# Kernel tuning notes

Hardware: AMD Instinct MI355X
Metric: run time of the kernel (lower is better)

The kernel has to match this reference:

```python
import jax, jax.numpy as jnp
import numpy as np

BS, NQ, DIMS = 4, 6400, 256
NH, NL, NP, NQUEUE = 8, 1, 4, 2


def ms_deform_attn(value, shapes_np, starts_np, loc, attn):
    # value: [B, Nv, H, D]; loc: [B, Nq, H, L, P, 2] in [0,1]; attn: [B, Nq, H, L, P]
    B, Nv, H, D = value.shape
    _, Nq, _, L, P, _ = loc.shape
    out = jnp.zeros((B, H, Nq, D), loc.dtype)
    for l in range(L):
        Hl, Wl = int(shapes_np[l, 0]), int(shapes_np[l, 1])
        s = int(starts_np[l])
        vl = value[:, s:s + Hl * Wl].transpose(0, 2, 1, 3)  # [B,H,HW,D]
        # grid_sample align_corners=False pixel coords
        x = loc[:, :, :, l, :, 0] * Wl - 0.5  # [B,Nq,H,P]
        y = loc[:, :, :, l, :, 1] * Hl - 0.5
        x0 = jnp.floor(x); y0 = jnp.floor(y)
        dx = x - x0; dy = y - y0
        x0i = x0.astype(jnp.int32); y0i = y0.astype(jnp.int32)
        acc = jnp.zeros((B, H, Nq * P, D), loc.dtype)
        corners = [(x0i, y0i, (1 - dx) * (1 - dy)),
                   (x0i + 1, y0i, dx * (1 - dy)),
                   (x0i, y0i + 1, (1 - dx) * dy),
                   (x0i + 1, y0i + 1, dx * dy)]
        for xi, yi, w in corners:
            valid = (xi >= 0) & (xi < Wl) & (yi >= 0) & (yi < Hl)
            idx = jnp.clip(yi, 0, Hl - 1) * Wl + jnp.clip(xi, 0, Wl - 1)  # [B,Nq,H,P]
            idx_t = idx.transpose(0, 2, 1, 3).reshape(B, H, Nq * P, 1)
            g = jnp.take_along_axis(vl, idx_t, axis=2)  # [B,H,Nq*P,D]
            wv = jnp.where(valid, w, 0.0).transpose(0, 2, 1, 3).reshape(B, H, Nq * P, 1)
            acc = acc + g * wv
        acc = acc.reshape(B, H, Nq, P, D)
        wl = attn[:, :, :, l].transpose(0, 2, 1, 3)  # [B,H,Nq,P]
        out = out + jnp.einsum('bhnpd,bhnp->bhnd', acc, wl)
    return out.transpose(0, 2, 1, 3).reshape(B, Nq, H * D)


def setup_inputs() -> dict:
    key = jax.random.key(0)
    ks = jax.random.split(key, 12)
    d2 = DIMS * NQUEUE
    noff = NQUEUE * NH * NL * NP * 2
    nattn = NQUEUE * NH * NL * NP
    sc = 1.0 / np.sqrt(DIMS)
    return {
        'query': jax.random.normal(ks[0], (BS, NQ, DIMS), jnp.float32),
        'voxbev': jax.random.normal(ks[1], (BS, NQ, DIMS), jnp.float32),
        'reference_points': jax.random.uniform(ks[2], (BS * NQUEUE, NQ, NL, 2), jnp.float32),
        'spatial_shapes': jnp.array([[80, 80]], dtype=jnp.int64),
        'level_start_index': jnp.array([0], dtype=jnp.int64),
        'Wv': jax.random.normal(ks[3], (DIMS, DIMS), jnp.float32) * sc,
        'bv': jax.random.normal(ks[4], (DIMS,), jnp.float32) * 0.01,
        'Woff': jax.random.normal(ks[5], (d2, noff), jnp.float32) * (1.0 / np.sqrt(d2)),
        'boff': jax.random.normal(ks[6], (noff,), jnp.float32),
        'Wattn': jax.random.normal(ks[7], (d2, nattn), jnp.float32) * (1.0 / np.sqrt(d2)),
        'battn': jax.random.normal(ks[8], (nattn,), jnp.float32) * 0.01,
        'Wo': jax.random.normal(ks[9], (DIMS, DIMS), jnp.float32) * sc,
        'bo': jax.random.normal(ks[10], (DIMS,), jnp.float32) * 0.01,
    }


def reference(query, voxbev, reference_points, spatial_shapes, level_start_index,
              Wv, bv, Woff, boff, Wattn, battn, Wo, bo):
    bs, nq, dims = query.shape
    shapes_np = np.asarray(spatial_shapes)
    starts_np = np.asarray(level_start_index)
    identity = query
    # value = stack([query, voxbev], 1).reshape(bs*2, nq, dims) -> interleaved [q0,v0,q1,v1,...]
    value = jnp.stack([query, voxbev], 1).reshape(bs * NQUEUE, nq, dims)
    qcat = jnp.concatenate([value[:bs], query], -1)  # [bs, nq, 2*dims]
    v = (value @ Wv + bv).reshape(bs * NQUEUE, nq, NH, dims // NH)
    off = (qcat @ Woff + boff).reshape(bs, nq, NH, NQUEUE, NL, NP, 2)
    attn = (qcat @ Wattn + battn).reshape(bs, nq, NH, NQUEUE, NL * NP)
    attn = jax.nn.softmax(attn, axis=-1).reshape(bs, nq, NH, NQUEUE, NL, NP)
    attn = attn.transpose(0, 3, 1, 2, 4, 5).reshape(bs * NQUEUE, nq, NH, NL, NP)
    off = off.transpose(0, 3, 1, 2, 4, 5, 6).reshape(bs * NQUEUE, nq, NH, NL, NP, 2)
    # offset normalizer: (W, H) per level
    norm = jnp.stack([spatial_shapes[:, 1], spatial_shapes[:, 0]], -1).astype(off.dtype)  # [L,2]
    loc = reference_points[:, :, None, :, None, :] + off / norm[None, None, None, :, None, :]
    out = ms_deform_attn(v, shapes_np, starts_np, loc, attn)  # [bs*2, nq, dims]
    out = out.reshape(bs, NQUEUE, nq, dims).mean(1)  # mean over queue
    out = out @ Wo + bo
    return out + identity  # dropout is identity in eval
```

## Files before the change

kernel.cpp:

```cpp
#include <hip/hip_runtime.h>
#include <hip/hip_bf16.h>

#define BS   4
#define NQ   6400
#define DIMS 256
#define NH   8
#define NP   4
#define GW   80
#define GH   80

typedef __hip_bfloat16 bf16;
typedef unsigned short ushort;
typedef __attribute__((ext_vector_type(8))) short short8;
typedef __attribute__((ext_vector_type(4))) float floatx4;

union bfu { bf16 h; ushort s; };
__device__ __forceinline__ ushort f2bs(float x) { bfu u; u.h = __float2bfloat16(x); return u.s; }
__device__ __forceinline__ float bs2f(ushort s) { return __uint_as_float(((unsigned)s) << 16); }
__device__ __forceinline__ float ldin(const void* p, size_t i, int isf) {
    return isf ? ((const float*)p)[i] : bs2f(((const ushort*)p)[i]);
}

__device__ __forceinline__ int self_detect(const ushort* __restrict__ q, int tid) {
    int bad = 0;
    const uint4 u0 = ((const uint4*)q)[tid * 2];
    const uint4 u1 = ((const uint4*)q)[tid * 2 + 1];
    const unsigned w[8] = { u0.x, u0.y, u0.z, u0.w, u1.x, u1.y, u1.z, u1.w };
    #pragma unroll
    for (int j = 0; j < 8; ++j) {
        if (((w[j] >> 7)  & 0xFF) > 160) bad = 1;
        if (((w[j] >> 23) & 0xFF) > 160) bad = 1;
    }
    return __any(bad) ? 1 : 0;
}

__global__ __launch_bounds__(256) void prep_k(
    const void* __restrict__ Wv, const void* __restrict__ bv,
    const void* __restrict__ Woff, const void* __restrict__ boff,
    const void* __restrict__ Wattn, const void* __restrict__ battn,
    const void* __restrict__ Wo, const void* __restrict__ bo,
    int* __restrict__ flagp,
    ushort* __restrict__ WvT, ushort* __restrict__ WoaT, ushort* __restrict__ WoT,
    float* __restrict__ biasv, float* __restrict__ biasoa, float* __restrict__ biaso,
    const void* __restrict__ query, const void* __restrict__ voxbev,
    uint4* __restrict__ qb, uint4* __restrict__ vbv)
{
    const int tid = threadIdx.x;
    const int isf = self_detect((const ushort*)query, tid);
    const int bid = blockIdx.x;
    if (bid == 0 && tid == 0) *flagp = isf;
    if (bid < 899) {
        const int i = bid * 256 + tid;
        const int n1 = 256 * 256, n2 = n1 + 192 * 512, n3 = n2 + 256 * 256;
        const int n4 = n3 + 256, n5 = n4 + 192, n6 = n5 + 256;
        if (i < n1) {
            int n = i >> 8, k = i & 255;
            WvT[i] = f2bs(ldin(Wv, (size_t)k * 256 + n, isf));
        } else if (i < n2) {
            int j = i - n1, n = j >> 9, k = j & 511;
            float v = (n < 128) ? ldin(Woff, (size_t)k * 128 + n, isf)
                                : ldin(Wattn, (size_t)k * 64 + (n - 128), isf);
            WoaT[j] = f2bs(v);
        } else if (i < n3) {
            int j = i - n2, n = j >> 8, k = j & 255;
            WoT[j] = f2bs(ldin(Wo, (size_t)k * 256 + n, isf));
        } else if (i < n4) {
            biasv[i - n3] = ldin(bv, i - n3, isf);
        } else if (i < n5) {
            int j = i - n4;
            biasoa[j] = (j < 128) ? ldin(boff, j, isf) : ldin(battn, j - 128, isf);
        } else if (i < n6) {
            biaso[i - n5] = ldin(bo, i - n5, isf);
        }
    } else {
        if (isf == 0) return;
        const int t = (bid - 899) * 256 + tid;
        const int half = 819200;
        const void* src = (t < half) ? query : voxbev;
        uint4* dst = (t < half) ? qb : vbv;
        const int j = (t < half) ? t : t - half;
        const float4* s = (const float4*)src + (size_t)j * 2;
        float4 a = s[0], b = s[1];
        uint4 o;
        o.x = ((unsigned)f2bs(a.y) << 16) | f2bs(a.x);
        o.y = ((unsigned)f2bs(a.w) << 16) | f2bs(a.z);
        o.z = ((unsigned)f2bs(b.y) << 16) | f2bs(b.x);
        o.w = ((unsigned)f2bs(b.w) << 16) | f2bs(b.z);
        dst[j] = o;
    }
}

enum { A_VAL = 0, A_QCAT = 1, A_PLAIN = 2 };
enum { O_BF16 = 0, O_FINAL = 1, O_VPERM = 2, O_OAPERM = 3 };

#define SROW 264
#define APAD 40
#define CST  67
#define SMEMB (64 * SROW * 2 + 2 * 128 * APAD * 2)

template <int AMODE, int OMODE, int KTOT, int NX, int MG>
__device__ __forceinline__ void pgemm_body(
    const int F, char* smem,
    const ushort* __restrict__ Apl, const ushort* __restrict__ BT,
    const float* __restrict__ biasf, void* __restrict__ C,
    const void* __restrict__ query_raw, const void* __restrict__ voxbev_raw,
    const ushort* __restrict__ qb, const ushort* __restrict__ vbv,
    const int isf)
{
    constexpr int N = NX * 64;
    constexpr int NPH = KTOT / 256;
    short* pan = (short*)smem;
    short* ap0 = (short*)(smem + 64 * SROW * 2);
    short* ap1 = ap0 + 128 * APAD;
    float* cbf = (float*)smem;

    const int xcd = F & 7, l = F >> 3;
    const int n = l % NX;
    const int mg = (l / NX) * 8 + xcd;
    if (mg >= MG) return;
    const int bm = mg * 128, bn = n * 64;

    const int tid = threadIdx.x;
    const int lane = tid & 63, wv = tid >> 6;
    const int wm = wv * 32;
    const int fr = lane & 15, fq = (lane >> 4) * 8;
    const int arow = tid >> 1, acs = (tid & 1) * 16;

    const ushort* qsrc = isf ? qb  : (const ushort*)query_raw;
    const ushort* vsrc = isf ? vbv : (const ushort*)voxbev_raw;
    const ushort* aph[NPH];
    if (AMODE == A_PLAIN) {
        aph[0] = Apl + (size_t)bm * DIMS;
    } else {
        const int b = bm / NQ, q0 = bm - (bm / NQ) * NQ;
        aph[0] = ((b & 1) ? vsrc : qsrc) + (size_t)((b >> 1) * NQ + q0) * DIMS;
        if (AMODE == A_QCAT) aph[1] = qsrc + (size_t)(b * NQ + q0) * DIMS;
    }

    floatx4 acc[2][4] = {};

    for (int ph = 0; ph < NPH; ++ph) {
        #pragma unroll
        for (int i = 0; i < 8; ++i) {
            const int c = tid * 8 + i;
            const int row = c >> 5, j = (c & 31) * 8;
            *(uint4*)&pan[row * SROW + j] =
                *(const uint4*)&BT[(size_t)(bn + row) * KTOT + ph * 256 + j];
        }
        const ushort* ab = aph[ph];
        {
            uint4 s0 = *(const uint4*)&ab[(size_t)arow * DIMS + acs];
            uint4 s1 = *(const uint4*)&ab[(size_t)arow * DIMS + acs + 8];
            *(uint4*)&ap0[arow * APAD + acs] = s0;
            *(uint4*)&ap0[arow * APAD + acs + 8] = s1;
        }
        __syncthreads();

        #pragma unroll
        for (int t = 0; t < 8; ++t) {
            const short* acur = (t & 1) ? ap1 : ap0;
            short* anxt = (t & 1) ? ap0 : ap1;
            uint4 s0, s1;
            if (t < 7) {
                s0 = *(const uint4*)&ab[(size_t)arow * DIMS + (t + 1) * 32 + acs];
                s1 = *(const uint4*)&ab[(size_t)arow * DIMS + (t + 1) * 32 + acs + 8];
            }
            short8 af[2], bf[4];
            #pragma unroll
            for (int mt = 0; mt < 2; ++mt)
                af[mt] = *(const short8*)&acur[(wm + mt * 16 + fr) * APAD + fq];
            #pragma unroll
            for (int nt = 0; nt < 4; ++nt)
                bf[nt] = *(const short8*)&pan[(nt * 16 + fr) * SROW + t * 32 + fq];
            #pragma unroll
            for (int mt = 0; mt < 2; ++mt)
                #pragma unroll
                for (int nt = 0; nt < 4; ++nt)
                    acc[mt][nt] = __builtin_amdgcn_mfma_f32_16x16x32_bf16(
                        af[mt], bf[nt], acc[mt][nt], 0, 0, 0);
            if (t < 7) {
                *(uint4*)&anxt[arow * APAD + acs] = s0;
                *(uint4*)&anxt[arow * APAD + acs + 8] = s1;
            }
            __syncthreads();
        }
    }

    const int col = lane & 15, rq = (lane >> 4) * 4;
    #pragma unroll
    for (int mt = 0; mt < 2; ++mt)
        #pragma unroll
        for (int nt = 0; nt < 4; ++nt)
            #pragma unroll
            for (int r = 0; r < 4; ++r)
                cbf[(wm + mt * 16 + rq + r) * CST + nt * 16 + col] = acc[mt][nt][r];
    __syncthreads();

    if (OMODE == O_FINAL && isf) {
        const int r16 = tid >> 4, cc = tid & 15;
        #pragma unroll
        for (int it = 0; it < 8; ++it) {
            const int lr = it * 16 + r16;
            const size_t g = (size_t)(bm + lr);
            float4 x = *(const float4*)&cbf[lr * CST + cc * 4];
            const ushort* rs = qsrc + g * DIMS + bn + cc * 4;
            x.x += biasf[bn + cc * 4 + 0] + bs2f(rs[0]);
            x.y += biasf[bn + cc * 4 + 1] + bs2f(rs[1]);
            x.z += biasf[bn + cc * 4 + 2] + bs2f(rs[2]);
            x.w += biasf[bn + cc * 4 + 3] + bs2f(rs[3]);
            *(float4*)((float*)C + g * N + bn + cc * 4) = x;
        }
    } else {
        const int r8 = tid >> 3, c8 = tid & 7;
        #pragma unroll
        for (int it = 0; it < 4; ++it) {
            const int lr = it * 32 + r8;
            const size_t g = (size_t)(bm + lr);
            float4 x0 = *(const float4*)&cbf[lr * CST + c8 * 8];
            float4 x1 = *(const float4*)&cbf[lr * CST + c8 * 8 + 4];
            float xs[8] = { x0.x, x0.y, x0.z, x0.w, x1.x, x1.y, x1.z, x1.w };
            #pragma unroll
            for (int e = 0; e < 8; ++e) xs[e] += biasf[bn + c8 * 8 + e];
            if (OMODE == O_FINAL) {
                const ushort* rs = qsrc + g * DIMS + bn + c8 * 8;
                #pragma unroll
                for (int e = 0; e < 8; ++e) xs[e] += bs2f(rs[e]);
            }
            uint4 o;
            o.x = ((unsigned)f2bs(xs[1]) << 16) | f2bs(xs[0]);
            o.y = ((unsigned)f2bs(xs[3]) << 16) | f2bs(xs[2]);
            o.z = ((unsigned)f2bs(xs[5]) << 16) | f2bs(xs[4]);
            o.w = ((unsigned)f2bs(xs[7]) << 16) | f2bs(xs[6]);
            ushort* dstp;
            if (OMODE == O_VPERM) {
                const int cc = bn + c8 * 8;
                const int s = (int)(g / NQ), qq = (int)(g % NQ);
                dstp = (ushort*)C + ((size_t)(s * 8 + (cc >> 5)) * NQ + qq) * 32
                                  + (cc & 31);
            } else if (OMODE == O_OAPERM) {
                const int cc = bn + c8 * 8;
                const int bb = (int)(g / NQ), qq = (int)(g % NQ);
                int hh, off;
                if (cc < 128) { hh = cc >> 4; off = cc & 15; }
                else          { hh = (cc - 128) >> 3; off = 16; }
                dstp = (ushort*)C + ((size_t)(bb * 8 + hh) * NQ + qq) * 24 + off;
            } else {
                dstp = (ushort*)C + g * N + bn + c8 * 8;
            }
            *(uint4*)dstp = o;
        }
    }
}

__global__ __launch_bounds__(256) void gemm12_k(
    const ushort* __restrict__ WvT, const float* __restrict__ biasv,
    ushort* __restrict__ v_ws,
    const ushort* __restrict__ WoaT, const float* __restrict__ biasoa,
    ushort* __restrict__ offraw,
    const void* __restrict__ query_raw, const void* __restrict__ voxbev_raw,
    const ushort* __restrict__ qb, const ushort* __restrict__ vbv,
    const int* __restrict__ flagp)
{
    __shared__ __align__(16) char smem[SMEMB];
    const int isf = *flagp;
    const int bid = blockIdx.x;
    if (bid < 1600) {
        pgemm_body<A_VAL, O_VPERM, 256, 4, 400>(bid, smem,
            nullptr, WvT, biasv, (void*)v_ws, query_raw, voxbev_raw, qb, vbv, isf);
    } else {
        pgemm_body<A_QCAT, O_OAPERM, 512, 3, 200>(bid - 1600, smem,
            nullptr, WoaT, biasoa, (void*)offraw, query_raw, voxbev_raw, qb, vbv, isf);
    }
}

__global__ __launch_bounds__(256) void gemm4_k(
    const ushort* __restrict__ Apl, const ushort* __restrict__ BT,
    const float* __restrict__ biasf, void* __restrict__ C,
    const void* __restrict__ query_raw, const void* __restrict__ voxbev_raw,
    const ushort* __restrict__ qb, const ushort* __restrict__ vbv,
    const int* __restrict__ flagp)
{
    __shared__ __align__(16) char smem[SMEMB];
    const int isf = *flagp;
    pgemm_body<A_PLAIN, O_FINAL, 256, 4, 200>(blockIdx.x, smem,
        Apl, BT, biasf, C, query_raw, voxbev_raw, qb, vbv, isf);
}

__global__ __launch_bounds__(256) void sample_k(
    const ushort* __restrict__ v,
    const ushort* __restrict__ offp,
    const void* __restrict__ refpts,
    const int* __restrict__ flagp,
    ushort* __restrict__ sampled)
{
    const int isf = *flagp;
    __shared__ int   sidx[64][2][17];
    __shared__ float swt [64][2][17];
    const int tid = threadIdx.x;
    const int j = blockIdx.x;
    const int h = j & 7;
    const int k = j >> 3;
    const int b = k / 100;
    const int q0 = (k % 100) * 64;

    if (tid < 128) {
        const int lq = tid >> 1, queue = tid & 1;
        const int q = q0 + lq;
        const ushort* rec = offp + ((size_t)(b * 8 + h) * NQ + q) * 24;
        const ushort* al = rec + 16 + queue * 4;
        float l0 = bs2f(al[0]), l1 = bs2f(al[1]), l2 = bs2f(al[2]), l3 = bs2f(al[3]);
        float mx = fmaxf(fmaxf(l0, l1), fmaxf(l2, l3));
        float e0 = __expf(l0 - mx), e1 = __expf(l1 - mx);
        float e2 = __expf(l2 - mx), e3 = __expf(l3 - mx);
        float inv = 0.5f / (e0 + e1 + e2 + e3);
        const int bq = b * 2 + queue;
        const float rx = ldin(refpts, ((size_t)bq * NQ + q) * 2 + 0, isf);
        const float ry = ldin(refpts, ((size_t)bq * NQ + q) * 2 + 1, isf);
        const ushort* od = rec + queue * 8;
        float ww[4] = { e0 * inv, e1 * inv, e2 * inv, e3 * inv };
        #pragma unroll
        for (int p = 0; p < NP; ++p) {
            const float x = rx * (float)GW + bs2f(od[p * 2 + 0]) - 0.5f;
            const float y = ry * (float)GH + bs2f(od[p * 2 + 1]) - 0.5f;
            const float x0f = floorf(x), y0f = floorf(y);
            const float dx = x - x0f, dy = y - y0f;
            const int x0 = (int)x0f, y0 = (int)y0f;
            const float wp = ww[p];
            const float cw4[4] = { wp * (1.0f - dx) * (1.0f - dy),
                                   wp * dx * (1.0f - dy),
                                   wp * (1.0f - dx) * dy,
                                   wp * dx * dy };
            #pragma unroll
            for (int c = 0; c < 4; ++c) {
                const int xs = x0 + (c & 1), ys = y0 + (c >> 1);
                const bool ok = (unsigned)xs < (unsigned)GW && (unsigned)ys < (unsigned)GH;
                const int xi = min(max(xs, 0), GW - 1);
                const int yi = min(max(ys, 0), GH - 1);
                sidx[lq][queue][p * 4 + c] = yi * GW + xi;
                swt [lq][queue][p * 4 + c] = ok ? cw4[c] : 0.0f;
            }
        }
    }
    __syncthreads();

    const int lq = tid >> 2, d8 = tid & 3;
    const int q = q0 + lq;
    float a[8] = {};
    #pragma unroll
    for (int queue = 0; queue < 2; ++queue) {
        const ushort* vb = v + (((size_t)(b * 2 + queue) * 8 + h) * NQ) * 32 + d8 * 8;
        #pragma unroll
        for (int hf = 0; hf < 2; ++hf) {
            uint4 g[8];
            #pragma unroll
            for (int u = 0; u < 8; ++u) {
                const int ci = sidx[lq][queue][hf * 8 + u];
                g[u] = *(const uint4*)&vb[(size_t)ci * 32];
            }
            __builtin_amdgcn_sched_barrier(0);
            #pragma unroll
            for (int u = 0; u < 8; ++u) {
                const float cw = swt[lq][queue][hf * 8 + u];
                a[0] += cw * bs2f((ushort)g[u].x); a[1] += cw * bs2f((ushort)(g[u].x >> 16));
                a[2] += cw * bs2f((ushort)g[u].y); a[3] += cw * bs2f((ushort)(g[u].y >> 16));
                a[4] += cw * bs2f((ushort)g[u].z); a[5] += cw * bs2f((ushort)(g[u].z >> 16));
                a[6] += cw * bs2f((ushort)g[u].w); a[7] += cw * bs2f((ushort)(g[u].w >> 16));
            }
        }
    }
    uint4 o;
    o.x = ((unsigned)f2bs(a[1]) << 16) | f2bs(a[0]);
    o.y = ((unsigned)f2bs(a[3]) << 16) | f2bs(a[2]);
    o.z = ((unsigned)f2bs(a[5]) << 16) | f2bs(a[4]);
    o.w = ((unsigned)f2bs(a[7]) << 16) | f2bs(a[6]);
    *(uint4*)&sampled[((size_t)b * NQ + q) * DIMS + h * 32 + d8 * 8] = o;
}

extern "C" void kernel_launch(void* const* d_in, const int* in_sizes, int n_in,
                              void* d_out, int out_size, void* d_ws, size_t ws_size,
                              hipStream_t stream)
{
    const void* query  = d_in[0];
    const void* voxbev = d_in[1];
    const void* refpts = d_in[2];
    const void* Wv   = d_in[5];  const void* bv    = d_in[6];
    const void* Woff = d_in[7];  const void* boff  = d_in[8];
    const void* Wattn= d_in[9];  const void* battn = d_in[10];
    const void* Wo   = d_in[11]; const void* bo    = d_in[12];

    char* p = (char*)d_ws;
    int* flag = (int*)p;             p += 256;
    ushort* WvT  = (ushort*)p;       p += 256 * 256 * 2;
    ushort* WoaT = (ushort*)p;       p += 192 * 512 * 2;
    ushort* WoT  = (ushort*)p;       p += 256 * 256 * 2;
    float* biasv  = (float*)p;       p += 1024;
    float* biasoa = (float*)p;       p += 1024;
    float* biaso  = (float*)p;       p += 1024;
    ushort* qb   = (ushort*)p;       p += (size_t)BS * NQ * DIMS * 2;
    ushort* vbv  = (ushort*)p;       p += (size_t)BS * NQ * DIMS * 2;
    ushort* v_ws = (ushort*)p;       p += (size_t)2 * BS * NQ * DIMS * 2;
    ushort* offraw = (ushort*)p;     p += (size_t)BS * NQ * 192 * 2;
    ushort* sampled = (ushort*)p;

    prep_k<<<7299, 256, 0, stream>>>(Wv, bv, Woff, boff, Wattn, battn, Wo, bo,
                                     flag, WvT, WoaT, WoT, biasv, biasoa, biaso,
                                     query, voxbev, (uint4*)qb, (uint4*)vbv);

    gemm12_k<<<2200, 256, 0, stream>>>(WvT, biasv, v_ws, WoaT, biasoa, offraw,
                                       query, voxbev, qb, vbv, flag);

    sample_k<<<3200, 256, 0, stream>>>(v_ws, offraw, refpts, flag, sampled);

    gemm4_k<<<800, 256, 0, stream>>>(sampled, WoT, biaso, d_out,
                                     query, voxbev, qb, vbv, flag);
}
```

Before: 209.7 us.

## Load GEMM tiles directly to LDS with XOR-swizzled layout and larger K tiles

```diff
diff --git a/kernel.cpp b/kernel.cpp
--- a/kernel.cpp
+++ b/kernel.cpp
@@ -19,6 +19,13 @@
 __device__ __forceinline__ float bs2f(ushort s) { return __uint_as_float(((unsigned)s) << 16); }
 __device__ __forceinline__ float ldin(const void* p, size_t i, int isf) {
     return isf ? ((const float*)p)[i] : bs2f(((const ushort*)p)[i]);
+}
+
+__device__ __forceinline__ void gl_lds16(const void* gsrc, void* ldst) {
+    __builtin_amdgcn_global_load_lds(
+        (const __attribute__((address_space(1))) unsigned int*)gsrc,
+        (__attribute__((address_space(3))) unsigned int*)ldst,
+        16, 0, 0);
 }
 
 __device__ __forceinline__ int self_detect(const ushort* __restrict__ q, int tid) {
@@ -93,10 +100,11 @@
 enum { A_VAL = 0, A_QCAT = 1, A_PLAIN = 2 };
 enum { O_BF16 = 0, O_FINAL = 1, O_VPERM = 2, O_OAPERM = 3 };
 
-#define SROW 264
-#define APAD 40
+#define BKS  128
+#define ABYT (128 * 256)
+#define BBYT (64 * 256)
 #define CST  67
-#define SMEMB (64 * SROW * 2 + 2 * 128 * APAD * 2)
+#define SMEMB (ABYT + BBYT)
 
 template <int AMODE, int OMODE, int KTOT, int NX, int MG>
 __device__ __forceinline__ void pgemm_body(
@@ -108,10 +116,9 @@
     const int isf)
 {
     constexpr int N = NX * 64;
-    constexpr int NPH = KTOT / 256;
-    short* pan = (short*)smem;
-    short* ap0 = (short*)(smem + 64 * SROW * 2);
-    short* ap1 = ap0 + 128 * APAD;
+    constexpr int NT = KTOT / BKS;
+    char* abuf = smem;
+    char* bbuf = smem + ABYT;
     float* cbf = (float*)smem;
 
     const int xcd = F & 7, l = F >> 3;
@@ -123,12 +130,13 @@
     const int tid = threadIdx.x;
     const int lane = tid & 63, wv = tid >> 6;
     const int wm = wv * 32;
-    const int fr = lane & 15, fq = (lane >> 4) * 8;
-    const int arow = tid >> 1, acs = (tid & 1) * 16;
+    const int fr = lane & 15;
+    const int srow = lane >> 4;
+    const int sslot = lane & 15;
 
     const ushort* qsrc = isf ? qb  : (const ushort*)query_raw;
     const ushort* vsrc = isf ? vbv : (const ushort*)voxbev_raw;
-    const ushort* aph[NPH];
+    const ushort* aph[2] = { nullptr, nullptr };
     if (AMODE == A_PLAIN) {
         aph[0] = Apl + (size_t)bm * DIMS;
     } else {
@@ -139,53 +147,55 @@
 
     floatx4 acc[2][4] = {};
 
-    for (int ph = 0; ph < NPH; ++ph) {
-        #pragma unroll
-        for (int i = 0; i < 8; ++i) {
-            const int c = tid * 8 + i;
-            const int row = c >> 5, j = (c & 31) * 8;
-            *(uint4*)&pan[row * SROW + j] =
-                *(const uint4*)&BT[(size_t)(bn + row) * KTOT + ph * 256 + j];
-        }
-        const ushort* ab = aph[ph];
-        {
-            uint4 s0 = *(const uint4*)&ab[(size_t)arow * DIMS + acs];
-            uint4 s1 = *(const uint4*)&ab[(size_t)arow * DIMS + acs + 8];
-            *(uint4*)&ap0[arow * APAD + acs] = s0;
-            *(uint4*)&ap0[arow * APAD + acs + 8] = s1;
-        }
+    #pragma unroll
+    for (int t = 0; t < NT; ++t) {
+        if (t > 0) __syncthreads();
+        #pragma unroll
+        for (int c8 = 0; c8 < 8; ++c8) {
+            const int c = wv * 8 + c8;
+            const int row = c * 4 + srow;
+            const int g = sslot ^ (row & 15);
+            const int k = t * BKS + g * 8;
+            const ushort* gp;
+            if (AMODE == A_QCAT && KTOT == 512)
+                gp = aph[k >> 8] + (size_t)row * DIMS + (k & 255);
+            else
+                gp = aph[0] + (size_t)row * DIMS + k;
+            gl_lds16(gp, abuf + c * 1024);
+        }
+        #pragma unroll
+        for (int c4 = 0; c4 < 4; ++c4) {
+            const int c = wv * 4 + c4;
+            const int row = c * 4 + srow;
+            const int g = sslot ^ (row & 15);
+            gl_lds16(&BT[(size_t)(bn + row) * KTOT + t * BKS + g * 8],
+                     bbuf + c * 1024);
+        }
+        asm volatile("s_waitcnt vmcnt(0)" ::: "memory");
         __syncthreads();
 
         #pragma unroll
-        for (int t = 0; t < 8; ++t) {
-            const short* acur = (t & 1) ? ap1 : ap0;
-            short* anxt = (t & 1) ? ap0 : ap1;
-            uint4 s0, s1;
-            if (t < 7) {
-                s0 = *(const uint4*)&ab[(size_t)arow * DIMS + (t + 1) * 32 + acs];
-                s1 = *(const uint4*)&ab[(size_t)arow * DIMS + (t + 1) * 32 + acs + 8];
-            }
+        for (int k0 = 0; k0 < BKS; k0 += 32) {
+            const int gl = (k0 >> 3) + (lane >> 4);
             short8 af[2], bf[4];
             #pragma unroll
             for (int mt = 0; mt < 2; ++mt)
-                af[mt] = *(const short8*)&acur[(wm + mt * 16 + fr) * APAD + fq];
+                af[mt] = *(const short8*)(abuf + (wm + mt * 16 + fr) * 256
+                                               + ((gl ^ fr) * 16));
             #pragma unroll
             for (int nt = 0; nt < 4; ++nt)
-                bf[nt] = *(const short8*)&pan[(nt * 16 + fr) * SROW + t * 32 + fq];
+                bf[nt] = *(const short8*)(bbuf + (nt * 16 + fr) * 256
+                                               + ((gl ^ fr) * 16));
             #pragma unroll
             for (int mt = 0; mt < 2; ++mt)
                 #pragma unroll
                 for (int nt = 0; nt < 4; ++nt)
                     acc[mt][nt] = __builtin_amdgcn_mfma_f32_16x16x32_bf16(
                         af[mt], bf[nt], acc[mt][nt], 0, 0, 0);
-            if (t < 7) {
-                *(uint4*)&anxt[arow * APAD + acs] = s0;
-                *(uint4*)&anxt[arow * APAD + acs + 8] = s1;
-            }
-            __syncthreads();
-        }
-    }
-
+        }
+    }
+
+    __syncthreads();
     const int col = lane & 15, rq = (lane >> 4) * 4;
     #pragma unroll
     for (int mt = 0; mt < 2; ++mt)
```

After: 182.7 us. 12.9% less time.
